# Kernel optimization log

Measured on AMD Instinct MI355X. Metric: run time of the kernel, lower is better.

Reference implementation:

```python
import jax, jax.numpy as jnp
import numpy as np

NX = 1024
N_HEAD = 16
HEAD_DIM = NX // N_HEAD
RPE_MAX = 20
LN_EPS = 1e-5


def _layernorm(h, g, b, eps=LN_EPS):
    mu = jnp.mean(h, axis=-1, keepdims=True)
    var = jnp.var(h, axis=-1, keepdims=True)
    return (h - mu) * jax.lax.rsqrt(var + eps) * g + b


def setup_inputs() -> dict:
    key = jax.random.key(0)
    ks = jax.random.split(key, 12)
    B, S = 2, 1024
    x = jax.random.normal(ks[0], (B, S, NX), dtype=jnp.float32)
    local_info = jax.random.normal(ks[1], (B, S, NX), dtype=jnp.float32)
    attention_mask = jnp.zeros((B, 1, 1, S), dtype=jnp.float32)
    pairwise_dist = jax.random.randint(ks[2], (B, S, S), -RPE_MAX, RPE_MAX + 1, dtype=jnp.int32)
    s = 0.02
    Wqkv = jax.random.normal(ks[3], (NX, 3 * NX), dtype=jnp.float32) * s
    bqkv = jnp.zeros((3 * NX,), dtype=jnp.float32)
    Wproj = jax.random.normal(ks[4], (NX, NX), dtype=jnp.float32) * s
    bproj = jnp.zeros((NX,), dtype=jnp.float32)
    rpek = jax.random.normal(ks[5], (2 * RPE_MAX + 1, HEAD_DIM), dtype=jnp.float32) * s
    ln1_g = jnp.ones((NX,), dtype=jnp.float32)
    ln1_b = jnp.zeros((NX,), dtype=jnp.float32)
    gate_W = jax.random.normal(ks[6], (2 * NX, NX), dtype=jnp.float32) * s
    return {"x": x, "local_info": local_info, "attention_mask": attention_mask,
            "pairwise_dist": pairwise_dist, "Wqkv": Wqkv, "bqkv": bqkv,
            "Wproj": Wproj, "bproj": bproj, "rpek": rpek,
            "ln1_g": ln1_g, "ln1_b": ln1_b, "gate_W": gate_W}


def reference(x, local_info, attention_mask, pairwise_dist, Wqkv, bqkv, Wproj, bproj, rpek, ln1_g, ln1_b, gate_W):
    B, S, _ = x.shape
    qkv = x @ Wqkv + bqkv                      # [B,S,3*NX]
    q, k, v = jnp.split(qkv, 3, axis=-1)
    q = q.reshape(B, S, N_HEAD, HEAD_DIM)
    k = k.reshape(B, S, N_HEAD, HEAD_DIM)
    v = v.reshape(B, S, N_HEAD, HEAD_DIM)
    # content scores [B,H,Q,K]
    w = jnp.einsum('bqhd,bkhd->bhqk', q, k)
    # relative-position bias: embedding lookup + per-query matmul
    k_rpe = rpek[pairwise_dist + RPE_MAX]      # [B,Q,K,D]
    w_rpe = jnp.einsum('bqhd,bqkd->bhqk', q, k_rpe)
    w = (w + w_rpe) / jnp.float32(HEAD_DIM) ** 0.5
    w = w + attention_mask
    p = jax.nn.softmax(w, axis=-1)
    a = jnp.einsum('bhqk,bkhd->bqhd', p, v).reshape(B, S, NX)
    a = a @ Wproj + bproj
    # residual + LN1
    h = _layernorm(x + a, ln1_g, ln1_b)
    # gated fusion of local and global info
    z = jax.nn.sigmoid(jnp.concatenate([local_info, h], axis=-1) @ gate_W)
    out = (1.0 - z) * h + z * local_info
    return out
```

## Files before the change

kernel.cpp:

```cpp
#include <hip/hip_runtime.h>
#include <hip/hip_bf16.h>

#define SEQ 1024
#define NH 16
#define HD 64
#define NXD 1024

typedef unsigned short u16;
typedef unsigned char u8;
typedef __attribute__((ext_vector_type(8))) short short8;
typedef __attribute__((ext_vector_type(4))) float f32x4;

__device__ __forceinline__ u16 f2bf(float f) {
    __hip_bfloat16 h = __float2bfloat16(f);
    u16 u; __builtin_memcpy(&u, &h, 2); return u;
}
__device__ __forceinline__ float bf2f(u16 u) {
    __hip_bfloat16 h; __builtin_memcpy(&h, &u, 2); return __bfloat162float(h);
}

__device__ __forceinline__ void gld16(const void* g, void* l) {
    __builtin_amdgcn_global_load_lds(
        (const __attribute__((address_space(1))) void*)g,
        (__attribute__((address_space(3))) void*)l, 16, 0, 0);
}

__device__ __forceinline__ void transpose_tile(const float* __restrict__ src,
        u16* __restrict__ dst, int R, int C, int bx, int by) {
    __shared__ float tile[32][33];
    int r0 = by * 32, c0 = bx * 32;
    int tr = threadIdx.x >> 3, tc = (threadIdx.x & 7) * 4;
    float4 v = *(const float4*)(src + (size_t)(r0 + tr) * C + c0 + tc);
    tile[tr][tc+0] = v.x; tile[tr][tc+1] = v.y; tile[tr][tc+2] = v.z; tile[tr][tc+3] = v.w;
    __syncthreads();
    u16* d = dst + (size_t)(c0 + tr) * R + r0 + tc;
    #pragma unroll
    for (int j = 0; j < 4; j++) d[j] = f2bf(tile[tc+j][tr]);
}

__global__ __launch_bounds__(256) void prep_all(const float* __restrict__ x,
        const float* __restrict__ local, const int* __restrict__ pd,
        const float* __restrict__ Wqkv, const float* __restrict__ Wproj,
        const float* __restrict__ gateW,
        u16* __restrict__ xb, u16* __restrict__ gateA, u8* __restrict__ pdu8,
        u16* __restrict__ WqkvT, u16* __restrict__ WprojT, u16* __restrict__ gateWT) {
    int bid = blockIdx.x;
    if (bid < 2048) {
        int i = (bid * 256 + threadIdx.x) * 4;
        float4 v = *(const float4*)(x + i);
        xb[i+0] = f2bf(v.x); xb[i+1] = f2bf(v.y); xb[i+2] = f2bf(v.z); xb[i+3] = f2bf(v.w);
    } else if (bid < 4096) {
        int i = ((bid - 2048) * 256 + threadIdx.x) * 4;
        int row = i >> 10, c = i & 1023;
        float4 v = *(const float4*)(local + i);
        u16* d = gateA + (size_t)row * 2048 + c;
        d[0] = f2bf(v.x); d[1] = f2bf(v.y); d[2] = f2bf(v.z); d[3] = f2bf(v.w);
    } else if (bid < 6144) {
        int i = ((bid - 4096) * 256 + threadIdx.x) * 4;
        int4 v = *(const int4*)(pd + i);
        uchar4 o;
        o.x = (u8)(v.x + 20); o.y = (u8)(v.y + 20);
        o.z = (u8)(v.z + 20); o.w = (u8)(v.w + 20);
        *(uchar4*)(pdu8 + i) = o;
    } else if (bid < 9216) {
        int k = bid - 6144;  transpose_tile(Wqkv,  WqkvT,  1024, 3072, k % 96, k / 96);
    } else if (bid < 10240) {
        int k = bid - 9216;  transpose_tile(Wproj, WprojT, 1024, 1024, k % 32, k / 32);
    } else {
        int k = bid - 10240; transpose_tile(gateW, gateWT, 2048, 1024, k % 32, k / 32);
    }
}

__global__ __launch_bounds__(256) void trq_kernel(const u16* __restrict__ vb,
        u16* __restrict__ vTb, const u16* __restrict__ qb,
        const float* __restrict__ rpek, u16* __restrict__ qrpe16) {
    int bid = blockIdx.x;
    if (bid < 2048) {
        __shared__ u16 tile[32][33];
        int bh = bid >> 6, d0 = ((bid >> 5) & 1) * 32, s0 = (bid & 31) * 32;
        int tr = threadIdx.x >> 3, tc = (threadIdx.x & 7) * 4;
        const u16* s = vb + ((size_t)bh * SEQ + s0 + tr) * HD + d0 + tc;
        #pragma unroll
        for (int j = 0; j < 4; j++) tile[tr][tc+j] = s[j];
        __syncthreads();
        u16* d = vTb + ((size_t)bh * HD + d0 + tr) * SEQ + s0 + tc;
        #pragma unroll
        for (int j = 0; j < 4; j++) d[j] = tile[tc+j][tr];
    } else {
        int t = threadIdx.x, lane = t & 63, wid = t >> 6;
        int quad = lane >> 4, l16 = lane & 15;
        int r0 = ((bid - 2048) * 4 + wid) * 16;
        short8 af[2];
        #pragma unroll
        for (int s = 0; s < 2; s++)
            af[s] = *(const short8*)(qb + (size_t)(r0 + l16) * HD + s * 32 + quad * 8);
        #pragma unroll
        for (int nt = 0; nt < 3; nt++) {
            int n = nt * 16 + l16;
            const float* rp = rpek + (size_t)(n < 41 ? n : 40) * HD;
            f32x4 acc = {0.f, 0.f, 0.f, 0.f};
            #pragma unroll
            for (int s = 0; s < 2; s++) {
                float4 f0 = *(const float4*)(rp + s * 32 + quad * 8);
                float4 f1 = *(const float4*)(rp + s * 32 + quad * 8 + 4);
                short8 bf;
                bf[0] = (short)f2bf(f0.x); bf[1] = (short)f2bf(f0.y);
                bf[2] = (short)f2bf(f0.z); bf[3] = (short)f2bf(f0.w);
                bf[4] = (short)f2bf(f1.x); bf[5] = (short)f2bf(f1.y);
                bf[6] = (short)f2bf(f1.z); bf[7] = (short)f2bf(f1.w);
                acc = __builtin_amdgcn_mfma_f32_16x16x32_bf16(af[s], bf, acc, 0, 0, 0);
            }
            if (n < 41) {
                #pragma unroll
                for (int r = 0; r < 4; r++)
                    qrpe16[(size_t)(r0 + quad * 4 + r) * 48 + n] = f2bf(acc[r]);
            }
        }
    }
}

template<int BM, int BN, int BK, int MBC, int NBC, int EPI>
__global__ __launch_bounds__(256) void gemm_bt(
        const u16* __restrict__ A, int lda, const u16* __restrict__ BT, int K,
        const float* __restrict__ bias, float* __restrict__ out_f,
        u16* __restrict__ oq, u16* __restrict__ ok, u16* __restrict__ ov,
        const u16* __restrict__ h16, const float* __restrict__ loc32,
        float* __restrict__ outg) {
    const int LOGBM = (BM == 128) ? 7 : 6;
    const int LOGBN = (BN == 128) ? 7 : 6;
    const int MT = BM / 32, NT = BN / 32, KS = BK / 32;
    __shared__ u16 Al[(BK / 8) * BM * 8];
    __shared__ u16 Bl[(BK / 8) * BN * 8];
    int t = threadIdx.x, lane = t & 63, wid = t >> 6;
    int quad = lane >> 4, l16 = lane & 15;
    int id = blockIdx.x;
    int xcd = id & 7, j = id >> 3;
    const int MPX = MBC / 8;
    int m0 = (xcd * MPX + j / NBC) * BM;
    int n0 = (j % NBC) * BN;
    int waveM = wid >> 1, waveN = wid & 1;
    f32x4 acc[MT][NT] = {};
    for (int k0 = 0; k0 < K; k0 += BK) {
        __syncthreads();
        #pragma unroll
        for (int i = 0; i < BM * BK / 2048; i++) {
            int c = t + i * 256, c0 = c & ~63;
            int m = c & (BM - 1), kb = c >> LOGBM;
            gld16(A + (size_t)(m0 + m) * lda + k0 + kb * 8,
                  &Al[((c0 >> LOGBM) * BM + (c0 & (BM - 1))) * 8]);
        }
        #pragma unroll
        for (int i = 0; i < BN * BK / 2048; i++) {
            int c = t + i * 256, c0 = c & ~63;
            int n = c & (BN - 1), kb = c >> LOGBN;
            gld16(BT + (size_t)(n0 + n) * K + k0 + kb * 8,
                  &Bl[((c0 >> LOGBN) * BN + (c0 & (BN - 1))) * 8]);
        }
        __syncthreads();
        short8 af[MT][KS], bfr[NT][KS];
        #pragma unroll
        for (int s = 0; s < KS; s++) {
            #pragma unroll
            for (int mt = 0; mt < MT; mt++)
                af[mt][s] = *(short8*)&Al[((s * 4 + quad) * BM + waveM * (BM / 2) + mt * 16 + l16) * 8];
            #pragma unroll
            for (int nt = 0; nt < NT; nt++)
                bfr[nt][s] = *(short8*)&Bl[((s * 4 + quad) * BN + waveN * (BN / 2) + nt * 16 + l16) * 8];
        }
        #pragma unroll
        for (int mt = 0; mt < MT; mt++)
            #pragma unroll
            for (int nt = 0; nt < NT; nt++)
                #pragma unroll
                for (int s = 0; s < KS; s++)
                    acc[mt][nt] = __builtin_amdgcn_mfma_f32_16x16x32_bf16(af[mt][s], bfr[nt][s], acc[mt][nt], 0, 0, 0);
    }
    #pragma unroll
    for (int mt = 0; mt < MT; mt++)
        #pragma unroll
        for (int nt = 0; nt < NT; nt++)
            #pragma unroll
            for (int r = 0; r < 4; r++) {
                int row = m0 + waveM * (BM / 2) + mt * 16 + quad * 4 + r;
                int col = n0 + waveN * (BN / 2) + nt * 16 + l16;
                float val = acc[mt][nt][r];
                if (EPI == 0) {
                    val += bias[col];
                    int b = row >> 10, s = row & 1023;
                    int sec = col >> 10, cc = col & 1023;
                    int h = cc >> 6, d = cc & 63;
                    u16 bv = f2bf(val);
                    size_t qidx = (((size_t)(b * NH + h)) * SEQ + s) * HD + d;
                    if (sec == 0)      oq[qidx] = bv;
                    else if (sec == 1) ok[qidx] = bv;
                    else               ov[qidx] = bv;
                } else if (EPI == 1) {
                    out_f[(size_t)row * 1024 + col] = val + bias[col];
                } else {
                    float z = 1.f / (1.f + __expf(-val));
                    size_t idx = (size_t)row * 1024 + col;
                    float hv = bf2f(h16[(size_t)row * 2048 + 1024 + col]);
                    outg[idx] = (1.f - z) * hv + z * loc32[idx];
                }
            }
}

__global__ __launch_bounds__(256) void attn_kernel(
        const u16* __restrict__ qb, const u16* __restrict__ kmat,
        const u16* __restrict__ vTb, const u16* __restrict__ qrpe16,
        const u8* __restrict__ pdu8, const float* __restrict__ mask,
        u16* __restrict__ po0, u16* __restrict__ po1, float* __restrict__ pl) {
    __shared__ u16 Kl[8 * 64 * 8];
    __shared__ u16 Vl[8 * 64 * 8];
    __shared__ u16 Pl[4][8 * 16 * 8];
    __shared__ u16 qr_lds[64 * 48];
    __shared__ u8 pdl[64 * 80];
    int t = threadIdx.x, lane = t & 63, wid = t >> 6;
    int quad = lane >> 4, l16 = lane & 15;

    int id = blockIdx.x;
    int xcd = id & 7, j = id >> 3;
    int b = xcd >> 2;
    int head = ((xcd & 3) << 2) | (j >> 5);
    int qblk = ((j >> 1) & 15) << 6;
    int sp = j & 1;
    int bh = (b << 4) | head;
    int q0 = qblk + wid * 16;

    {
        const u16* src = qrpe16 + ((size_t)bh * SEQ + qblk) * 48;
        { int c = t, c0 = c & ~63; gld16(src + (size_t)c * 8, &qr_lds[c0 * 8]); }
        if (wid < 2) { int c = 256 + t, c0 = c & ~63; gld16(src + (size_t)c * 8, &qr_lds[c0 * 8]); }
    }

    short8 aq[2];
    #pragma unroll
    for (int s = 0; s < 2; s++)
        aq[s] = *(const short8*)(qb + ((size_t)bh * SEQ + q0 + l16) * HD + s * 32 + quad * 8);
    f32x4 o[4] = {};
    float lrow[4] = {0.f, 0.f, 0.f, 0.f};
    u16* Pw = Pl[wid];
    const u8* pdbase = pdu8 + ((size_t)b * SEQ + qblk) * SEQ;
    for (int kt = 0; kt < 8; kt++) {
        int k0 = sp * 512 + kt * 64;
        __syncthreads();
        #pragma unroll
        for (int i = 0; i < 2; i++) {
            int c = t + i * 256, c0 = c & ~63;
            int s = c & 63, g = c >> 6, g0 = c0 >> 6;
            gld16(kmat + ((size_t)bh * SEQ + k0 + s) * HD + g * 8, &Kl[(g0 * 64) * 8]);
            gld16(vTb + ((size_t)bh * HD + s) * SEQ + k0 + g * 8, &Vl[(g0 * 64) * 8]);
        }
        {
            int qrow = t >> 2, kj = (t & 3) * 16;
            uint4 pv = *(const uint4*)(pdbase + (size_t)qrow * SEQ + k0 + kj);
            *(uint4*)&pdl[qrow * 80 + kj] = pv;
        }
        __syncthreads();
        #pragma unroll
        for (int ks = 0; ks < 4; ks++) {
            f32x4 a = {0.f, 0.f, 0.f, 0.f};
            #pragma unroll
            for (int dh = 0; dh < 2; dh++) {
                short8 bk = *(short8*)&Kl[((dh * 4 + quad) * 64 + ks * 16 + l16) * 8];
                a = __builtin_amdgcn_mfma_f32_16x16x32_bf16(aq[dh], bk, a, 0, 0, 0);
            }
            int kcol = k0 + ks * 16 + l16;
            float mk = mask[b * SEQ + kcol];
            int kcl = ks * 16 + l16;
            #pragma unroll
            for (int r = 0; r < 4; r++) {
                int ql = wid * 16 + quad * 4 + r;
                int pdv = pdl[ql * 80 + kcl];
                float rpe = bf2f(qr_lds[ql * 48 + pdv]);
                float sc = (a[r] + rpe) * 0.125f + mk;
                float p = __expf(fminf(sc, 30.f));
                lrow[r] += p;
                Pw[((kcl >> 3) * 16 + quad * 4 + r) * 8 + (kcl & 7)] = f2bf(p);
            }
        }
        asm volatile("s_waitcnt lgkmcnt(0)" ::: "memory");
        #pragma unroll
        for (int ks2 = 0; ks2 < 2; ks2++) {
            short8 pa = *(short8*)&Pw[((ks2 * 4 + quad) * 16 + l16) * 8];
            #pragma unroll
            for (int dt = 0; dt < 4; dt++) {
                short8 vv = *(short8*)&Vl[((ks2 * 4 + quad) * 64 + dt * 16 + l16) * 8];
                o[dt] = __builtin_amdgcn_mfma_f32_16x16x32_bf16(pa, vv, o[dt], 0, 0, 0);
            }
        }
    }
    #pragma unroll
    for (int r = 0; r < 4; r++) {
        #pragma unroll
        for (int off = 1; off < 16; off <<= 1)
            lrow[r] += __shfl_xor(lrow[r], off, 16);
    }
    u16* po = sp ? po1 : po0;
    #pragma unroll
    for (int r = 0; r < 4; r++) {
        int row = bh * SEQ + q0 + quad * 4 + r;
        #pragma unroll
        for (int dt = 0; dt < 4; dt++)
            po[(size_t)row * 64 + dt * 16 + l16] = f2bf(o[dt][r]);
        if (l16 == 0)
            pl[sp * 32768 + row] = lrow[r];
    }
}

__global__ __launch_bounds__(256) void attn_combine(const u16* __restrict__ po0,
        const u16* __restrict__ po1, const float* __restrict__ pl,
        u16* __restrict__ aoutb) {
    int idx = blockIdx.x * 256 + threadIdx.x;
    int row = idx >> 6, d = idx & 63;
    float l0 = pl[row], l1 = pl[32768 + row];
    float inv = 1.f / (l0 + l1);
    float o0 = bf2f(po0[(size_t)row * 64 + d]);
    float o1 = bf2f(po1[(size_t)row * 64 + d]);
    float val = (o0 + o1) * inv;
    int bh = row >> 10, qrow = row & 1023;
    int b = bh >> 4, h = bh & 15;
    aoutb[((size_t)(b * SEQ + qrow)) * NXD + h * HD + d] = f2bf(val);
}

__device__ __forceinline__ float block_sum(float v, float* sred) {
    #pragma unroll
    for (int o = 32; o > 0; o >>= 1) v += __shfl_down(v, o, 64);
    int lane = threadIdx.x & 63, wid = threadIdx.x >> 6;
    __syncthreads();
    if (lane == 0) sred[wid] = v;
    __syncthreads();
    return sred[0] + sred[1] + sred[2] + sred[3];
}

__global__ __launch_bounds__(256) void ln_kernel(const float* __restrict__ x,
        const float* __restrict__ a, const float* __restrict__ g,
        const float* __restrict__ bln, u16* __restrict__ gateA) {
    int row = blockIdx.x;
    __shared__ float sred[4];
    float vals[4];
    float s = 0.f;
    #pragma unroll
    for (int i = 0; i < 4; i++) {
        int c = threadIdx.x + i * 256;
        vals[i] = x[(size_t)row * NXD + c] + a[(size_t)row * NXD + c];
        s += vals[i];
    }
    s = block_sum(s, sred);
    float mu = s * (1.f / NXD);
    float vs = 0.f;
    #pragma unroll
    for (int i = 0; i < 4; i++) { float d = vals[i] - mu; vs += d * d; }
    vs = block_sum(vs, sred);
    float rstd = rsqrtf(vs * (1.f / NXD) + 1e-5f);
    #pragma unroll
    for (int i = 0; i < 4; i++) {
        int c = threadIdx.x + i * 256;
        float hv = (vals[i] - mu) * rstd * g[c] + bln[c];
        gateA[(size_t)row * 2048 + 1024 + c] = f2bf(hv);
    }
}

extern "C" void kernel_launch(void* const* d_in, const int* in_sizes, int n_in,
                              void* d_out, int out_size, void* d_ws, size_t ws_size,
                              hipStream_t stream) {
    const float* x     = (const float*)d_in[0];
    const float* local = (const float*)d_in[1];
    const float* mask  = (const float*)d_in[2];
    const int*   pd    = (const int*)d_in[3];
    const float* Wqkv  = (const float*)d_in[4];
    const float* bqkv  = (const float*)d_in[5];
    const float* Wproj = (const float*)d_in[6];
    const float* bproj = (const float*)d_in[7];
    const float* rpek  = (const float*)d_in[8];
    const float* ln_g  = (const float*)d_in[9];
    const float* ln_b  = (const float*)d_in[10];
    const float* gateW = (const float*)d_in[11];
    float* out = (float*)d_out;

    char* ws = (char*)d_ws;
    const size_t MB = 1u << 20;
    u16*   xb    = (u16*)(ws + 0);
    u16*   WqkvT = (u16*)(ws + 4 * MB);
    u16*   po0   = (u16*)(ws + 4 * MB);
    float* pl    = (float*)(ws + 8 * MB);
    u16*   WprojT= (u16*)(ws + 10 * MB);
    u16*   qb    = (u16*)(ws + 12 * MB);
    u16*   kb    = (u16*)(ws + 16 * MB);
    u16*   vb    = (u16*)(ws + 20 * MB);
    u16*   po1   = (u16*)(ws + 20 * MB);
    float* pout  = (float*)(ws + 16 * MB);
    u16*   vTb   = (u16*)(ws + 24 * MB);
    u16*   qrpe16= (u16*)(ws + 28 * MB);
    u16*   gateA = (u16*)(ws + 34 * MB);
    u8*    pdu8  = (u8*)(ws + 42 * MB);
    u16*   gateWT= (u16*)(ws + 44 * MB);
    u16*   aoutb = xb;

    prep_all<<<12288, 256, 0, stream>>>(x, local, pd, Wqkv, Wproj, gateW,
            xb, gateA, pdu8, WqkvT, WprojT, gateWT);
    gemm_bt<64, 128, 64, 32, 24, 0><<<768, 256, 0, stream>>>(xb, 1024, WqkvT, 1024, bqkv,
            nullptr, qb, kb, vb, nullptr, nullptr, nullptr);
    trq_kernel<<<2560, 256, 0, stream>>>(vb, vTb, qb, rpek, qrpe16);
    attn_kernel<<<1024, 256, 0, stream>>>(qb, kb, vTb, qrpe16, pdu8, mask,
            po0, po1, pl);
    attn_combine<<<8192, 256, 0, stream>>>(po0, po1, pl, aoutb);
    gemm_bt<64, 64, 128, 32, 16, 1><<<512, 256, 0, stream>>>(aoutb, 1024, WprojT, 1024, bproj,
            pout, nullptr, nullptr, nullptr, nullptr, nullptr, nullptr);
    ln_kernel<<<2048, 256, 0, stream>>>(x, pout, ln_g, ln_b, gateA);
    gemm_bt<64, 64, 128, 32, 16, 2><<<512, 256, 0, stream>>>(gateA, 2048, gateWT, 2048, nullptr,
            nullptr, nullptr, nullptr, nullptr, gateA, local, out);
}
```

Measured before the change: 258.7 us.

## Fuse attention split-combine into projection GEMM A-tile load

Removes the separate attn_combine kernel: the projection GEMM now reads the two partial attention outputs and their softmax denominators directly, normalizes them and writes bf16 into the A tile in LDS. It also restructures the MFMA inner loop to load fragments per k-substep, and raises BK for the QKV GEMM to 128. This saves a launch and a full write and read of the intermediate activation, at the cost of synchronous, uncoalesced-ish loads in the GEMM prologue instead of async global-to-LDS loads.

```diff
diff --git a/kernel.cpp b/kernel.cpp
--- a/kernel.cpp
+++ b/kernel.cpp
@@ -125,7 +125,9 @@
         const float* __restrict__ bias, float* __restrict__ out_f,
         u16* __restrict__ oq, u16* __restrict__ ok, u16* __restrict__ ov,
         const u16* __restrict__ h16, const float* __restrict__ loc32,
-        float* __restrict__ outg) {
+        float* __restrict__ outg,
+        const u16* __restrict__ po0, const u16* __restrict__ po1,
+        const float* __restrict__ pl) {
     const int LOGBM = (BM == 128) ? 7 : 6;
     const int LOGBN = (BN == 128) ? 7 : 6;
     const int MT = BM / 32, NT = BN / 32, KS = BK / 32;
@@ -144,10 +146,27 @@
         __syncthreads();
         #pragma unroll
         for (int i = 0; i < BM * BK / 2048; i++) {
-            int c = t + i * 256, c0 = c & ~63;
+            int c = t + i * 256;
             int m = c & (BM - 1), kb = c >> LOGBM;
-            gld16(A + (size_t)(m0 + m) * lda + k0 + kb * 8,
-                  &Al[((c0 >> LOGBM) * BM + (c0 & (BM - 1))) * 8]);
+            if (EPI == 1) {
+                int row = m0 + m;
+                int b = row >> 10, s = row & 1023;
+                int kcol = k0 + kb * 8;
+                int h = kcol >> 6, d = kcol & 63;
+                size_t rowa = ((size_t)(b * NH + h)) * SEQ + s;
+                short8 v0 = *(const short8*)(po0 + rowa * 64 + d);
+                short8 v1 = *(const short8*)(po1 + rowa * 64 + d);
+                float inv = 1.f / (pl[rowa] + pl[32768 + rowa]);
+                short8 o8;
+                #pragma unroll
+                for (int e = 0; e < 8; e++)
+                    o8[e] = (short)f2bf((bf2f((u16)v0[e]) + bf2f((u16)v1[e])) * inv);
+                *(short8*)&Al[(kb * BM + m) * 8] = o8;
+            } else {
+                int c0 = c & ~63;
+                gld16(A + (size_t)(m0 + m) * lda + k0 + kb * 8,
+                      &Al[((c0 >> LOGBM) * BM + (c0 & (BM - 1))) * 8]);
+            }
         }
         #pragma unroll
         for (int i = 0; i < BN * BK / 2048; i++) {
@@ -157,23 +176,21 @@
                   &Bl[((c0 >> LOGBN) * BN + (c0 & (BN - 1))) * 8]);
         }
         __syncthreads();
-        short8 af[MT][KS], bfr[NT][KS];
         #pragma unroll
         for (int s = 0; s < KS; s++) {
+            short8 af[MT], bfr[NT];
             #pragma unroll
             for (int mt = 0; mt < MT; mt++)
-                af[mt][s] = *(short8*)&Al[((s * 4 + quad) * BM + waveM * (BM / 2) + mt * 16 + l16) * 8];
+                af[mt] = *(short8*)&Al[((s * 4 + quad) * BM + waveM * (BM / 2) + mt * 16 + l16) * 8];
             #pragma unroll
             for (int nt = 0; nt < NT; nt++)
-                bfr[nt][s] = *(short8*)&Bl[((s * 4 + quad) * BN + waveN * (BN / 2) + nt * 16 + l16) * 8];
-        }
-        #pragma unroll
-        for (int mt = 0; mt < MT; mt++)
-            #pragma unroll
-            for (int nt = 0; nt < NT; nt++)
+                bfr[nt] = *(short8*)&Bl[((s * 4 + quad) * BN + waveN * (BN / 2) + nt * 16 + l16) * 8];
+            #pragma unroll
+            for (int mt = 0; mt < MT; mt++)
                 #pragma unroll
-                for (int s = 0; s < KS; s++)
-                    acc[mt][nt] = __builtin_amdgcn_mfma_f32_16x16x32_bf16(af[mt][s], bfr[nt][s], acc[mt][nt], 0, 0, 0);
+                for (int nt = 0; nt < NT; nt++)
+                    acc[mt][nt] = __builtin_amdgcn_mfma_f32_16x16x32_bf16(af[mt], bfr[nt], acc[mt][nt], 0, 0, 0);
+        }
     }
     #pragma unroll
     for (int mt = 0; mt < MT; mt++)
@@ -308,21 +325,6 @@
     }
 }
 
-__global__ __launch_bounds__(256) void attn_combine(const u16* __restrict__ po0,
-        const u16* __restrict__ po1, const float* __restrict__ pl,
-        u16* __restrict__ aoutb) {
-    int idx = blockIdx.x * 256 + threadIdx.x;
-    int row = idx >> 6, d = idx & 63;
-    float l0 = pl[row], l1 = pl[32768 + row];
-    float inv = 1.f / (l0 + l1);
-    float o0 = bf2f(po0[(size_t)row * 64 + d]);
-    float o1 = bf2f(po1[(size_t)row * 64 + d]);
-    float val = (o0 + o1) * inv;
-    int bh = row >> 10, qrow = row & 1023;
-    int b = bh >> 4, h = bh & 15;
-    aoutb[((size_t)(b * SEQ + qrow)) * NXD + h * HD + d] = f2bf(val);
-}
-
 __device__ __forceinline__ float block_sum(float v, float* sred) {
     #pragma unroll
     for (int o = 32; o > 0; o >>= 1) v += __shfl_down(v, o, 64);
@@ -389,25 +391,23 @@
     u16*   kb    = (u16*)(ws + 16 * MB);
     u16*   vb    = (u16*)(ws + 20 * MB);
     u16*   po1   = (u16*)(ws + 20 * MB);
-    float* pout  = (float*)(ws + 16 * MB);
     u16*   vTb   = (u16*)(ws + 24 * MB);
     u16*   qrpe16= (u16*)(ws + 28 * MB);
     u16*   gateA = (u16*)(ws + 34 * MB);
     u8*    pdu8  = (u8*)(ws + 42 * MB);
     u16*   gateWT= (u16*)(ws + 44 * MB);
-    u16*   aoutb = xb;
+    float* pout  = (float*)(ws + 48 * MB);
 
     prep_all<<<12288, 256, 0, stream>>>(x, local, pd, Wqkv, Wproj, gateW,
             xb, gateA, pdu8, WqkvT, WprojT, gateWT);
-    gemm_bt<64, 128, 64, 32, 24, 0><<<768, 256, 0, stream>>>(xb, 1024, WqkvT, 1024, bqkv,
-            nullptr, qb, kb, vb, nullptr, nullptr, nullptr);
+    gemm_bt<64, 128, 128, 32, 24, 0><<<768, 256, 0, stream>>>(xb, 1024, WqkvT, 1024, bqkv,
+            nullptr, qb, kb, vb, nullptr, nullptr, nullptr, nullptr, nullptr, nullptr);
     trq_kernel<<<2560, 256, 0, stream>>>(vb, vTb, qb, rpek, qrpe16);
     attn_kernel<<<1024, 256, 0, stream>>>(qb, kb, vTb, qrpe16, pdu8, mask,
             po0, po1, pl);
-    attn_combine<<<8192, 256, 0, stream>>>(po0, po1, pl, aoutb);
-    gemm_bt<64, 64, 128, 32, 16, 1><<<512, 256, 0, stream>>>(aoutb, 1024, WprojT, 1024, bproj,
-            pout, nullptr, nullptr, nullptr, nullptr, nullptr, nullptr);
+    gemm_bt<64, 64, 128, 32, 16, 1><<<512, 256, 0, stream>>>(nullptr, 1024, WprojT, 1024, bproj,
+            pout, nullptr, nullptr, nullptr, nullptr, nullptr, nullptr, po0, po1, pl);
     ln_kernel<<<2048, 256, 0, stream>>>(x, pout, ln_g, ln_b, gateA);
     gemm_bt<64, 64, 128, 32, 16, 2><<<512, 256, 0, stream>>>(gateA, 2048, gateWT, 2048, nullptr,
-            nullptr, nullptr, nullptr, nullptr, gateA, local, out);
-}
+            nullptr, nullptr, nullptr, nullptr, gateA, local, out, nullptr, nullptr, nullptr);
+}
```

Result: slower. 269.3 us (+4.1%).
